# Kernel optimization log

Hardware: AMD Instinct MI355X
Metric: run time of the kernel (lower is better)

Reference implementation:

```python
import jax, jax.numpy as jnp
import numpy as np

B, S, D = 2, 2048, 4096
NH, NKV, HD = 32, 8, 128
NREP = NH // NKV
ROPE_THETA = 10000.0


def setup_inputs() -> dict:
    key = jax.random.key(0)
    k1, k2, k3, k4, k5 = jax.random.split(key, 5)
    x = jax.random.normal(k1, (B, S, D), jnp.float32)
    wq = jax.random.normal(k2, (NH * HD, D), jnp.float32) * 0.02
    wk = jax.random.normal(k3, (NKV * HD, D), jnp.float32) * 0.02
    wv = jax.random.normal(k4, (NKV * HD, D), jnp.float32) * 0.02
    wo = jax.random.normal(k5, (D, NH * HD), jnp.float32) * 0.02
    inv_freq = 1.0 / (ROPE_THETA ** (np.arange(0, HD, 2, dtype=np.float64) / HD))
    ang = np.outer(np.arange(S, dtype=np.float64), inv_freq)  # [S, HD/2]
    return {
        'x': x, 'start_pos': 0,
        'freqs_cos': jnp.asarray(np.cos(ang), jnp.float32),
        'freqs_sin': jnp.asarray(np.sin(ang), jnp.float32),
        'wq': wq, 'wk': wk, 'wv': wv, 'wo': wo,
    }


def _apply_rope(x, cos, sin):
    # x: [B, S, H, HD]; cos/sin: [S, HD/2]. Matches torch view_as_complex on
    # interleaved (even, odd) feature pairs: (xr + i*xi) * (cos + i*sin).
    xr = x[..., 0::2]
    xi = x[..., 1::2]
    c = cos[None, :, None, :]
    s = sin[None, :, None, :]
    out_r = xr * c - xi * s
    out_i = xr * s + xi * c
    return jnp.stack([out_r, out_i], axis=-1).reshape(x.shape)


def reference(x, start_pos, freqs_cos, freqs_sin, wq, wk, wv, wo):
    b, s, _ = x.shape
    xq = (x @ wq.T).reshape(b, s, NH, HD)
    xk = (x @ wk.T).reshape(b, s, NKV, HD)
    xv = (x @ wv.T).reshape(b, s, NKV, HD)
    # Source applies RoPE to K and V (not Q) -- reproduced faithfully.
    xk = _apply_rope(xk, freqs_cos, freqs_sin)
    xv = _apply_rope(xv, freqs_cos, freqs_sin)
    # start_pos == 0 prefill: cache slice [:, :start_pos+s] == freshly written xk/xv.
    # repeat_kv: head h_out = h_kv * NREP + rep  ==  jnp.repeat along head axis.
    keys = jnp.repeat(xk, NREP, axis=2)    # [B, S, NH, HD]
    values = jnp.repeat(xv, NREP, axis=2)  # [B, S, NH, HD]
    scale = 1.0 / jnp.sqrt(jnp.asarray(HD, x.dtype))
    scores = jnp.einsum('bqhd,bkhd->bhqk', xq, keys) * scale  # [B, NH, S, S]
    probs = jax.nn.softmax(scores, axis=-1)  # NOTE: no causal mask in source
    out = jnp.einsum('bhqk,bkhd->bqhd', probs, values).reshape(b, s, NH * HD)
    return out @ wo.T
```

## Files before the change

### kernel.cpp

```cpp
#include <hip/hip_runtime.h>
#include <hip/hip_bf16.h>


typedef short bf16x8 __attribute__((ext_vector_type(8)));
typedef float f32x4 __attribute__((ext_vector_type(4)));

__device__ __forceinline__ void load16(const void* g, void* l) {
  __builtin_amdgcn_global_load_lds(
      (const __attribute__((address_space(1))) void*)g,
      (__attribute__((address_space(3))) void*)l, 16, 0, 0);
}

__device__ __forceinline__ f32x4 mfma16(bf16x8 a, bf16x8 b, f32x4 c) {
  return __builtin_amdgcn_mfma_f32_16x16x32_bf16(a, b, c, 0, 0, 0);
}

__device__ __forceinline__ unsigned short f2b(float f) {
  union { float f; unsigned int u; } v; v.f = f;
  unsigned int u = v.u;
  return (unsigned short)((u + 0x7fffu + ((u >> 16) & 1u)) >> 16);
}
__device__ __forceinline__ float b2f(unsigned short u) {
  union { unsigned int u; float f; } v; v.u = ((unsigned int)u) << 16;
  return v.f;
}
__device__ __forceinline__ unsigned short f2b_fast(float f) {
  __hip_bfloat16 h = __float2bfloat16(f);
  return *reinterpret_cast<unsigned short*>(&h);
}

#define QSCALE (0.08838834764831845f * 1.4426950408889634f)

__global__ __launch_bounds__(256) void cvt_f32_bf16(
    const float* __restrict__ in, unsigned short* __restrict__ out, int n4) {
  int idx = blockIdx.x * 256 + threadIdx.x;
  int stride = gridDim.x * 256;
  for (int i = idx; i < n4; i += stride) {
    float4 v = reinterpret_cast<const float4*>(in)[i];
    ushort4 o;
    o.x = f2b(v.x); o.y = f2b(v.y); o.z = f2b(v.z); o.w = f2b(v.w);
    reinterpret_cast<ushort4*>(out)[i] = o;
  }
}

template <typename OutT>
__global__ __launch_bounds__(512, 2) void gemm256(
    const unsigned short* __restrict__ A, const unsigned short* __restrict__ Bw,
    OutT* __restrict__ C, int M, int N, int K, int sbl) {
  extern __shared__ char smem[];
  const int tid = threadIdx.x;
  const int lane = tid & 63;
  const int w = tid >> 6;
  const int lr = lane & 15, lg = lane >> 4;
  const int wr = w >> 2, wc = w & 3;

  const int nbn = N >> 8;
  const int bid = blockIdx.x, nwg = gridDim.x;
  const int swz = (bid & 7) * (nwg >> 3) + (bid >> 3);
  const int bm = swz / nbn, bn = swz % nbn;

  const unsigned short* Ag = A + (size_t)bm * 256 * K;
  const unsigned short* Bg = Bw + (size_t)bn * 256 * K;

  int srow[4], skhw[4], sdst[4];
#pragma unroll
  for (int j = 0; j < 4; ++j) {
    const int c = tid + j * 512;
    srow[j] = c >> 3;
    skhw[j] = ((c & 7) ^ ((c >> 3) & 7)) << 3;
    sdst[j] = ((tid & ~63) << 4) + j * 8192;
  }

  f32x4 acc[8][4];
#pragma unroll
  for (int m = 0; m < 8; ++m)
#pragma unroll
    for (int n = 0; n < 4; ++n) acc[m][n] = (f32x4){0.f, 0.f, 0.f, 0.f};

#define STAGEA4(tt)                                                           \
  {                                                                           \
    char* d = smem + (((tt)&1) * 65536);                                      \
    _Pragma("unroll") for (int j = 0; j < 4; ++j)                             \
        load16(Ag + (size_t)srow[j] * K + ((tt) << 6) + skhw[j], d + sdst[j]);\
  }
#define STAGEB4(tt)                                                           \
  {                                                                           \
    char* d = smem + (((tt)&1) * 65536) + 32768;                              \
    _Pragma("unroll") for (int j = 0; j < 4; ++j)                             \
        load16(Bg + (size_t)srow[j] * K + ((tt) << 6) + skhw[j], d + sdst[j]);\
  }

  STAGEB4(0);
  STAGEA4(0);

  const int NT = K >> 6;
  const int rx = (lr & 7) << 4;
  const int aRow0 = (wr * 128 + lr) * 128;
  const int bRow0 = (wc * 64 + lr) * 128;
  const int col0 = (lg * 16) ^ rx;
  const int col1 = (64 + lg * 16) ^ rx;

  bf16x8 aR[4][2], bR[4][2];

  for (int t = 0; t < NT; ++t) {
    const char* bufA = smem + (t & 1) * 65536;
    const char* bufB = bufA + 32768;
    const bool more = (t + 1) < NT;

    asm volatile("s_waitcnt vmcnt(0)" ::: "memory");
    __builtin_amdgcn_s_barrier();

#pragma unroll
    for (int mf = 0; mf < 4; ++mf) {
      aR[mf][0] = *(const bf16x8*)(bufA + aRow0 + mf * 2048 + col0);
      aR[mf][1] = *(const bf16x8*)(bufA + aRow0 + mf * 2048 + col1);
    }
#pragma unroll
    for (int nf = 0; nf < 2; ++nf) {
      bR[nf][0] = *(const bf16x8*)(bufB + bRow0 + nf * 2048 + col0);
      bR[nf][1] = *(const bf16x8*)(bufB + bRow0 + nf * 2048 + col1);
    }
    if (more) STAGEB4(t + 1);
    asm volatile("s_waitcnt lgkmcnt(8)" ::: "memory");
    __builtin_amdgcn_s_barrier();
    asm volatile("s_waitcnt lgkmcnt(0)" ::: "memory");
    __builtin_amdgcn_sched_barrier(0);
    __builtin_amdgcn_s_setprio(1);
#pragma unroll
    for (int mf = 0; mf < 4; ++mf)
#pragma unroll
      for (int nf = 0; nf < 2; ++nf) {
        acc[mf][nf] = mfma16(aR[mf][0], bR[nf][0], acc[mf][nf]);
        acc[mf][nf] = mfma16(aR[mf][1], bR[nf][1], acc[mf][nf]);
      }
    __builtin_amdgcn_s_setprio(0);
    __builtin_amdgcn_s_barrier();

#pragma unroll
    for (int nf = 2; nf < 4; ++nf) {
      bR[nf][0] = *(const bf16x8*)(bufB + bRow0 + nf * 2048 + col0);
      bR[nf][1] = *(const bf16x8*)(bufB + bRow0 + nf * 2048 + col1);
    }
    if (more) STAGEA4(t + 1);
    __builtin_amdgcn_s_barrier();
    asm volatile("s_waitcnt lgkmcnt(0)" ::: "memory");
    __builtin_amdgcn_sched_barrier(0);
    __builtin_amdgcn_s_setprio(1);
#pragma unroll
    for (int mf = 0; mf < 4; ++mf)
#pragma unroll
      for (int nf = 2; nf < 4; ++nf) {
        acc[mf][nf] = mfma16(aR[mf][0], bR[nf][0], acc[mf][nf]);
        acc[mf][nf] = mfma16(aR[mf][1], bR[nf][1], acc[mf][nf]);
      }
    __builtin_amdgcn_s_setprio(0);
    __builtin_amdgcn_s_barrier();

#pragma unroll
    for (int mf = 0; mf < 4; ++mf) {
      aR[mf][0] = *(const bf16x8*)(bufA + aRow0 + (4 + mf) * 2048 + col0);
      aR[mf][1] = *(const bf16x8*)(bufA + aRow0 + (4 + mf) * 2048 + col1);
    }
    __builtin_amdgcn_s_barrier();
    asm volatile("s_waitcnt lgkmcnt(0)" ::: "memory");
    __builtin_amdgcn_sched_barrier(0);
    __builtin_amdgcn_s_setprio(1);
#pragma unroll
    for (int mf = 0; mf < 4; ++mf)
#pragma unroll
      for (int nf = 0; nf < 2; ++nf) {
        acc[4 + mf][nf] = mfma16(aR[mf][0], bR[nf][0], acc[4 + mf][nf]);
        acc[4 + mf][nf] = mfma16(aR[mf][1], bR[nf][1], acc[4 + mf][nf]);
      }
    __builtin_amdgcn_s_setprio(0);
    __builtin_amdgcn_s_barrier();

    __builtin_amdgcn_s_setprio(1);
#pragma unroll
    for (int mf = 0; mf < 4; ++mf)
#pragma unroll
      for (int nf = 2; nf < 4; ++nf) {
        acc[4 + mf][nf] = mfma16(aR[mf][0], bR[nf][0], acc[4 + mf][nf]);
        acc[4 + mf][nf] = mfma16(aR[mf][1], bR[nf][1], acc[4 + mf][nf]);
      }
    __builtin_amdgcn_s_setprio(0);
  }
#undef STAGEA4
#undef STAGEB4

  const float cscale = (bn < sbl) ? QSCALE : 1.0f;
#pragma unroll
  for (int mf = 0; mf < 8; ++mf)
#pragma unroll
    for (int nf = 0; nf < 4; ++nf)
#pragma unroll
      for (int r = 0; r < 4; ++r) {
        int rowc = bm * 256 + wr * 128 + mf * 16 + lg * 4 + r;
        int colc = bn * 256 + wc * 64 + nf * 16 + lr;
        float v = acc[mf][nf][r] * cscale;
        if constexpr (sizeof(OutT) == 2)
          C[(size_t)rowc * N + colc] = (OutT)f2b(v);
        else
          C[(size_t)rowc * N + colc] = v;
      }
}

__global__ __launch_bounds__(256) void rope_kv(
    const unsigned short* __restrict__ XQKV,
    const float* __restrict__ fc, const float* __restrict__ fs,
    unsigned short* __restrict__ Kr, unsigned short* __restrict__ Vt) {
  __shared__ unsigned short Vl[128][66];
  const int t = threadIdx.x;
  const int bid = blockIdx.x;
  const int stile = bid & 31, bkv = bid >> 5;
  const int b = bkv >> 3, kvh = bkv & 7;
  const int s0 = stile * 64;
  const int l = t & 63;
  const int jrow = t >> 6;

  for (int j = 0; j < 16; ++j) {
    int s = s0 + j * 4 + jrow;
    ushort2 v = *(const ushort2*)(XQKV + (size_t)(b * 2048 + s) * 6144 + 4096 +
                                  kvh * 128 + 2 * l);
    float c = fc[s * 64 + l], sn = fs[s * 64 + l];
    float xr = b2f(v.x), xi = b2f(v.y);
    ushort2 o;
    o.x = f2b(xr * c - xi * sn);
    o.y = f2b(xr * sn + xi * c);
    *(ushort2*)(Kr + ((size_t)bkv * 2048 + s) * 128 + 2 * l) = o;
  }
  for (int j = 0; j < 16; ++j) {
    int ss = j * 4 + jrow;
    int s = s0 + ss;
    ushort2 v = *(const ushort2*)(XQKV + (size_t)(b * 2048 + s) * 6144 + 5120 +
                                  kvh * 128 + 2 * l);
    float c = fc[s * 64 + l], sn = fs[s * 64 + l];
    float xr = b2f(v.x), xi = b2f(v.y);
    Vl[2 * l][ss] = f2b(xr * c - xi * sn);
    Vl[2 * l + 1][ss] = f2b(xr * sn + xi * c);
  }
  __syncthreads();
  const int d = t >> 1, half = t & 1;
  unsigned short* vdst = Vt + ((size_t)bkv * 128 + d) * 2048 + s0 + half * 32;
#pragma unroll
  for (int e = 0; e < 32; e += 4) {
    ushort4 pk;
    pk.x = Vl[d][half * 32 + e];
    pk.y = Vl[d][half * 32 + e + 1];
    pk.z = Vl[d][half * 32 + e + 2];
    pk.w = Vl[d][half * 32 + e + 3];
    *(ushort4*)(vdst + e) = pk;
  }
}

__global__ __launch_bounds__(256, 2) void attn_fwd(
    const unsigned short* __restrict__ XQ, const unsigned short* __restrict__ Kr,
    const unsigned short* __restrict__ Vt, unsigned short* __restrict__ AO) {
  extern __shared__ char smem[];
  char* Ksm = smem;
  char* Vsm = smem + 16384;
  unsigned short* Ps = (unsigned short*)(smem + 32768);
  const int t = threadIdx.x;
  const int lane = t & 63, w = t >> 6;
  const int lr = lane & 15, lg = lane >> 4;

  const int bid = blockIdx.x;
  const int nwg = gridDim.x;
  const int swz = (bid & 7) * (nwg >> 3) + (bid >> 3);
  const int qt = swz & 7;
  const int bh = swz >> 3;
  const int b = bh >> 5, h = bh & 31;
  const int bkv = b * 8 + (h >> 2);

  bf16x8 qf[4][4];
#pragma unroll
  for (int q4 = 0; q4 < 4; ++q4) {
    const unsigned short* qp =
        XQ + ((size_t)(b * 2048 + qt * 256 + w * 64 + q4 * 16 + lr)) * 6144 +
        h * 128 + lg * 8;
#pragma unroll
    for (int dc = 0; dc < 4; ++dc) qf[q4][dc] = *(const bf16x8*)(qp + dc * 32);
  }

  f32x4 acc[4][8];
#pragma unroll
  for (int q4 = 0; q4 < 4; ++q4)
#pragma unroll
    for (int i = 0; i < 8; ++i) acc[q4][i] = (f32x4){0.f, 0.f, 0.f, 0.f};
  float l_[4][4];
#pragma unroll
  for (int q4 = 0; q4 < 4; ++q4)
#pragma unroll
    for (int r = 0; r < 4; ++r) l_[q4][r] = 0.f;

  const unsigned short* Kbase = Kr + (size_t)bkv * 2048 * 128;
  const unsigned short* Vbase = Vt + (size_t)bkv * 128 * 2048;

  const int c0 = t, c1 = t + 256;
  const int kK0 = c0 & 31, dC0 = c0 >> 5;
  const int kK1 = c1 & 31, dC1 = c1 >> 5;
  const int vD0 = c0 & 127, vKc0 = c0 >> 7;
  const int vD1 = c1 & 127, vKc1 = c1 >> 7;
  const int dstb0 = (c0 & ~63) * 16;
  const int dstb1 = (c1 & ~63) * 16;

#define STAGE_KV(bufi, kt)                                                     \
  {                                                                            \
    char* kd = Ksm + (bufi)*8192;                                              \
    char* vd = Vsm + (bufi)*8192;                                              \
    load16(Kbase + (size_t)((kt)*32 + kK0) * 128 + dC0 * 8, kd + dstb0);       \
    load16(Kbase + (size_t)((kt)*32 + kK1) * 128 + dC1 * 8, kd + dstb1);       \
    load16(Vbase + (size_t)vD0 * 2048 + (kt)*32 + vKc0 * 8, vd + dstb0);       \
    load16(Vbase + (size_t)vD1 * 2048 + (kt)*32 + vKc1 * 8, vd + dstb1);       \
  }

  STAGE_KV(0, 0);
  asm volatile("s_waitcnt vmcnt(0)" ::: "memory");
  __builtin_amdgcn_s_barrier();

  unsigned short* Pw = Ps + w * 2048;
  const int pbase = (lr >> 3) * 512 + (lr & 7);

  for (int kt = 0; kt < 64; ++kt) {
    const int cur = kt & 1;
    if (kt < 63) STAGE_KV(cur ^ 1, kt + 1);

    const char* Kc = Ksm + cur * 8192;
    const char* Vc = Vsm + cur * 8192;

#pragma unroll
    for (int nf = 0; nf < 2; ++nf) {
      f32x4 s[4];
#pragma unroll
      for (int q4 = 0; q4 < 4; ++q4) s[q4] = (f32x4){0.f, 0.f, 0.f, 0.f};
#pragma unroll
      for (int dc = 0; dc < 4; ++dc) {
        bf16x8 kf =
            *(const bf16x8*)(Kc + ((dc * 4 + lg) * 32 + nf * 16 + lr) * 16);
#pragma unroll
        for (int q4 = 0; q4 < 4; ++q4) s[q4] = mfma16(qf[q4][dc], kf, s[q4]);
      }
      const int pb = pbase + nf * 1024;
#pragma unroll
      for (int q4 = 0; q4 < 4; ++q4)
#pragma unroll
        for (int r = 0; r < 4; ++r) {
          float p = __builtin_amdgcn_exp2f(s[q4][r]);
          l_[q4][r] += p;
          Pw[pb + (q4 * 16 + lg * 4 + r) * 8] = f2b_fast(p);
        }
    }

    bf16x8 pf[4];
#pragma unroll
    for (int q4 = 0; q4 < 4; ++q4)
      pf[q4] = *(const bf16x8*)(Pw + lg * 512 + (q4 * 16 + lr) * 8);
#pragma unroll
    for (int dt = 0; dt < 8; ++dt) {
      bf16x8 vf = *(const bf16x8*)(Vc + (lg * 128 + dt * 16 + lr) * 16);
#pragma unroll
      for (int q4 = 0; q4 < 4; ++q4)
        acc[q4][dt] = mfma16(pf[q4], vf, acc[q4][dt]);
    }

    asm volatile("s_waitcnt vmcnt(0)" ::: "memory");
    __builtin_amdgcn_s_barrier();
  }
#undef STAGE_KV

#pragma unroll
  for (int q4 = 0; q4 < 4; ++q4)
#pragma unroll
    for (int r = 0; r < 4; ++r) {
#pragma unroll
      for (int o = 1; o < 16; o <<= 1) l_[q4][r] += __shfl_xor(l_[q4][r], o);
    }

#pragma unroll
  for (int q4 = 0; q4 < 4; ++q4)
#pragma unroll
    for (int r = 0; r < 4; ++r) {
      float inv = 1.f / l_[q4][r];
      size_t rowb =
          ((size_t)(b * 2048 + qt * 256 + w * 64 + q4 * 16 + lg * 4 + r)) * 4096 +
          h * 128;
#pragma unroll
      for (int dt = 0; dt < 8; ++dt)
        AO[rowb + dt * 16 + lr] = f2b_fast(acc[q4][dt][r] * inv);
    }
}

extern "C" void kernel_launch(void* const* d_in, const int* in_sizes, int n_in,
                              void* d_out, int out_size, void* d_ws, size_t ws_size,
                              hipStream_t stream) {
  const float* x  = (const float*)d_in[0];
  const float* fc = (const float*)d_in[2];
  const float* fs = (const float*)d_in[3];
  const float* wq = (const float*)d_in[4];
  const float* wk = (const float*)d_in[5];
  const float* wv = (const float*)d_in[6];
  const float* wo = (const float*)d_in[7];

  const size_t MB = 1024ull * 1024ull;
  char* ws = (char*)d_ws;
  unsigned short* Xb   = (unsigned short*)(ws);
  unsigned short* Wsc  = (unsigned short*)(ws + 32 * MB);
  unsigned short* Kr   = (unsigned short*)(ws);
  unsigned short* Vt   = (unsigned short*)(ws + 8 * MB);
  unsigned short* AO   = (unsigned short*)(ws + 80 * MB);
  unsigned short* XQKV = (unsigned short*)d_out;

  (void)hipFuncSetAttribute((const void*)gemm256<unsigned short>,
                            hipFuncAttributeMaxDynamicSharedMemorySize, 131072);
  (void)hipFuncSetAttribute((const void*)gemm256<float>,
                            hipFuncAttributeMaxDynamicSharedMemorySize, 131072);
  (void)hipFuncSetAttribute((const void*)attn_fwd,
                            hipFuncAttributeMaxDynamicSharedMemorySize, 49152);

  dim3 blk(256);
  dim3 blk512(512);
  cvt_f32_bf16<<<2048, blk, 0, stream>>>(x, Xb, (2 * 2048 * 4096) / 4);
  cvt_f32_bf16<<<2048, blk, 0, stream>>>(wq, Wsc, (4096 * 4096) / 4);
  cvt_f32_bf16<<<2048, blk, 0, stream>>>(wk, Wsc + 4096 * 4096, (1024 * 4096) / 4);
  cvt_f32_bf16<<<2048, blk, 0, stream>>>(wv, Wsc + 5120 * 4096, (1024 * 4096) / 4);
  gemm256<unsigned short><<<384, blk512, 131072, stream>>>(
      Xb, Wsc, XQKV, 4096, 6144, 4096, 16);
  rope_kv<<<512, blk, 0, stream>>>(XQKV, fc, fs, Kr, Vt);
  attn_fwd<<<512, blk, 49152, stream>>>(XQKV, Kr, Vt, AO);
  cvt_f32_bf16<<<2048, blk, 0, stream>>>(wo, Wsc, (4096 * 4096) / 4);
  gemm256<float><<<256, blk512, 131072, stream>>>(
      AO, Wsc, (float*)d_out, 4096, 4096, 4096, 0);
}
```

Baseline: 564.7 us.

## Deepen GEMM prefetch pipeline with split-half staging and partial vmcnt waits

Rewrites the GEMM main loop to process two K-tiles per iteration. Global-to-LDS loads are split into half-tile chunks issued between MFMA phases, and the full vmcnt(0) drain is replaced with vmcnt(10) gates so more loads stay in flight. B rows are remapped so each wave's 32-column slices land contiguously in LDS halves. Redundant wraparound loads (te/to fallback to tiles 0/1) are issued at the end, and the layout reasoning is fragile: vmcnt counting and buffer reuse must be exactly right or results break.

Result: faster. 542.9 us (-3.9%).

```diff
diff --git a/kernel.cpp b/kernel.cpp
--- a/kernel.cpp
+++ b/kernel.cpp
@@ -62,131 +62,207 @@
   const unsigned short* Ag = A + (size_t)bm * 256 * K;
   const unsigned short* Bg = Bw + (size_t)bn * 256 * K;
 
-  int srow[4], skhw[4], sdst[4];
+  int aoffs[4], boffs[4], sdst[4];
 #pragma unroll
   for (int j = 0; j < 4; ++j) {
     const int c = tid + j * 512;
-    srow[j] = c >> 3;
-    skhw[j] = ((c & 7) ^ ((c >> 3) & 7)) << 3;
+    const int u = c >> 3;
+    const int slot = ((c & 7) ^ (u & 7)) << 3;
+    aoffs[j] = u * K + slot;
+    const int br = ((u & 127) >> 5) * 64 + (u >> 7) * 32 + (u & 31);
+    boffs[j] = br * K + slot;
     sdst[j] = ((tid & ~63) << 4) + j * 8192;
   }
 
-  f32x4 acc[8][4];
-#pragma unroll
-  for (int m = 0; m < 8; ++m)
-#pragma unroll
-    for (int n = 0; n < 4; ++n) acc[m][n] = (f32x4){0.f, 0.f, 0.f, 0.f};
-
-#define STAGEA4(tt)                                                           \
+#define ST_A(hh, tt)                                                          \
   {                                                                           \
     char* d = smem + (((tt)&1) * 65536);                                      \
-    _Pragma("unroll") for (int j = 0; j < 4; ++j)                             \
-        load16(Ag + (size_t)srow[j] * K + ((tt) << 6) + skhw[j], d + sdst[j]);\
-  }
-#define STAGEB4(tt)                                                           \
+    load16(Ag + aoffs[(hh)] + ((tt) << 6), d + sdst[(hh)]);                   \
+    load16(Ag + aoffs[(hh) + 2] + ((tt) << 6), d + sdst[(hh) + 2]);           \
+  }
+#define ST_B(hh, tt)                                                          \
   {                                                                           \
     char* d = smem + (((tt)&1) * 65536) + 32768;                              \
-    _Pragma("unroll") for (int j = 0; j < 4; ++j)                             \
-        load16(Bg + (size_t)srow[j] * K + ((tt) << 6) + skhw[j], d + sdst[j]);\
-  }
-
-  STAGEB4(0);
-  STAGEA4(0);
+    load16(Bg + boffs[(hh)*2] + ((tt) << 6), d + sdst[(hh)*2]);               \
+    load16(Bg + boffs[(hh)*2 + 1] + ((tt) << 6), d + sdst[(hh)*2 + 1]);       \
+  }
+#define GATE10                                                                \
+  asm volatile("s_waitcnt vmcnt(10)" ::: "memory");                           \
+  __builtin_amdgcn_s_barrier();
+#define LGKM0                                                                 \
+  asm volatile("s_waitcnt lgkmcnt(0)" ::: "memory");                          \
+  __builtin_amdgcn_sched_barrier(0);
+
+  f32x4 acc[8][4];
+#pragma unroll
+  for (int m = 0; m < 8; ++m)
+#pragma unroll
+    for (int n = 0; n < 4; ++n) acc[m][n] = (f32x4){0.f, 0.f, 0.f, 0.f};
+
+  ST_A(0, 0); ST_B(0, 0); ST_B(1, 0); ST_A(1, 0);
+  ST_A(0, 1); ST_B(0, 1); ST_B(1, 1);
 
   const int NT = K >> 6;
-  const int rx = (lr & 7) << 4;
-  const int aRow0 = (wr * 128 + lr) * 128;
-  const int bRow0 = (wc * 64 + lr) * 128;
-  const int col0 = (lg * 16) ^ rx;
-  const int col1 = (64 + lg * 16) ^ rx;
-
-  bf16x8 aR[4][2], bR[4][2];
-
-  for (int t = 0; t < NT; ++t) {
-    const char* bufA = smem + (t & 1) * 65536;
-    const char* bufB = bufA + 32768;
-    const bool more = (t + 1) < NT;
-
-    asm volatile("s_waitcnt vmcnt(0)" ::: "memory");
-    __builtin_amdgcn_s_barrier();
-
+  const int NI = NT >> 1;
+  const int xr = (lr & 7) << 4;
+  const int aBase = (wr * 128 + lr) * 128;
+  const int bBase = (wc * 32 + lr) * 128;
+  const int col0 = (lg * 16) ^ xr;
+  const int col1 = (64 + lg * 16) ^ xr;
+
+  bf16x8 aR[4][2], b01[2][2], b23[2][2];
+
+  for (int i = 0; i < NI; ++i) {
+    const int T1 = 2 * i + 1;
+    const int te = (2 * i + 2 < NT) ? 2 * i + 2 : 0;
+    const int to = (2 * i + 3 < NT) ? 2 * i + 3 : 1;
+    const char* d0 = smem;
+    const char* d1 = smem + 65536;
+
+    GATE10;
 #pragma unroll
     for (int mf = 0; mf < 4; ++mf) {
-      aR[mf][0] = *(const bf16x8*)(bufA + aRow0 + mf * 2048 + col0);
-      aR[mf][1] = *(const bf16x8*)(bufA + aRow0 + mf * 2048 + col1);
+      aR[mf][0] = *(const bf16x8*)(d0 + aBase + mf * 2048 + col0);
+      aR[mf][1] = *(const bf16x8*)(d0 + aBase + mf * 2048 + col1);
     }
 #pragma unroll
     for (int nf = 0; nf < 2; ++nf) {
-      bR[nf][0] = *(const bf16x8*)(bufB + bRow0 + nf * 2048 + col0);
-      bR[nf][1] = *(const bf16x8*)(bufB + bRow0 + nf * 2048 + col1);
-    }
-    if (more) STAGEB4(t + 1);
-    asm volatile("s_waitcnt lgkmcnt(8)" ::: "memory");
-    __builtin_amdgcn_s_barrier();
-    asm volatile("s_waitcnt lgkmcnt(0)" ::: "memory");
-    __builtin_amdgcn_sched_barrier(0);
-    __builtin_amdgcn_s_setprio(1);
-#pragma unroll
-    for (int mf = 0; mf < 4; ++mf)
-#pragma unroll
-      for (int nf = 0; nf < 2; ++nf) {
-        acc[mf][nf] = mfma16(aR[mf][0], bR[nf][0], acc[mf][nf]);
-        acc[mf][nf] = mfma16(aR[mf][1], bR[nf][1], acc[mf][nf]);
-      }
-    __builtin_amdgcn_s_setprio(0);
-    __builtin_amdgcn_s_barrier();
-
-#pragma unroll
-    for (int nf = 2; nf < 4; ++nf) {
-      bR[nf][0] = *(const bf16x8*)(bufB + bRow0 + nf * 2048 + col0);
-      bR[nf][1] = *(const bf16x8*)(bufB + bRow0 + nf * 2048 + col1);
-    }
-    if (more) STAGEA4(t + 1);
-    __builtin_amdgcn_s_barrier();
-    asm volatile("s_waitcnt lgkmcnt(0)" ::: "memory");
-    __builtin_amdgcn_sched_barrier(0);
-    __builtin_amdgcn_s_setprio(1);
-#pragma unroll
-    for (int mf = 0; mf < 4; ++mf)
-#pragma unroll
-      for (int nf = 2; nf < 4; ++nf) {
-        acc[mf][nf] = mfma16(aR[mf][0], bR[nf][0], acc[mf][nf]);
-        acc[mf][nf] = mfma16(aR[mf][1], bR[nf][1], acc[mf][nf]);
-      }
-    __builtin_amdgcn_s_setprio(0);
-    __builtin_amdgcn_s_barrier();
-
+      b01[nf][0] = *(const bf16x8*)(d0 + 32768 + bBase + nf * 2048 + col0);
+      b01[nf][1] = *(const bf16x8*)(d0 + 32768 + bBase + nf * 2048 + col1);
+    }
+    ST_A(1, T1);
+    LGKM0;
+    __builtin_amdgcn_s_setprio(1);
+#pragma unroll
+    for (int mf = 0; mf < 4; ++mf)
+#pragma unroll
+      for (int nf = 0; nf < 2; ++nf) {
+        acc[mf][nf] = mfma16(aR[mf][0], b01[nf][0], acc[mf][nf]);
+        acc[mf][nf] = mfma16(aR[mf][1], b01[nf][1], acc[mf][nf]);
+      }
+    __builtin_amdgcn_s_setprio(0);
+
+    GATE10;
+#pragma unroll
+    for (int nf = 0; nf < 2; ++nf) {
+      b23[nf][0] = *(const bf16x8*)(d0 + 32768 + 16384 + bBase + nf * 2048 + col0);
+      b23[nf][1] = *(const bf16x8*)(d0 + 32768 + 16384 + bBase + nf * 2048 + col1);
+    }
+    ST_A(0, te);
+    LGKM0;
+    __builtin_amdgcn_s_setprio(1);
+#pragma unroll
+    for (int mf = 0; mf < 4; ++mf)
+#pragma unroll
+      for (int nf = 0; nf < 2; ++nf) {
+        acc[mf][2 + nf] = mfma16(aR[mf][0], b23[nf][0], acc[mf][2 + nf]);
+        acc[mf][2 + nf] = mfma16(aR[mf][1], b23[nf][1], acc[mf][2 + nf]);
+      }
+    __builtin_amdgcn_s_setprio(0);
+
+    GATE10;
 #pragma unroll
     for (int mf = 0; mf < 4; ++mf) {
-      aR[mf][0] = *(const bf16x8*)(bufA + aRow0 + (4 + mf) * 2048 + col0);
-      aR[mf][1] = *(const bf16x8*)(bufA + aRow0 + (4 + mf) * 2048 + col1);
-    }
-    __builtin_amdgcn_s_barrier();
-    asm volatile("s_waitcnt lgkmcnt(0)" ::: "memory");
-    __builtin_amdgcn_sched_barrier(0);
-    __builtin_amdgcn_s_setprio(1);
-#pragma unroll
-    for (int mf = 0; mf < 4; ++mf)
-#pragma unroll
-      for (int nf = 0; nf < 2; ++nf) {
-        acc[4 + mf][nf] = mfma16(aR[mf][0], bR[nf][0], acc[4 + mf][nf]);
-        acc[4 + mf][nf] = mfma16(aR[mf][1], bR[nf][1], acc[4 + mf][nf]);
-      }
-    __builtin_amdgcn_s_setprio(0);
-    __builtin_amdgcn_s_barrier();
-
-    __builtin_amdgcn_s_setprio(1);
-#pragma unroll
-    for (int mf = 0; mf < 4; ++mf)
-#pragma unroll
-      for (int nf = 2; nf < 4; ++nf) {
-        acc[4 + mf][nf] = mfma16(aR[mf][0], bR[nf][0], acc[4 + mf][nf]);
-        acc[4 + mf][nf] = mfma16(aR[mf][1], bR[nf][1], acc[4 + mf][nf]);
-      }
-    __builtin_amdgcn_s_setprio(0);
-  }
-#undef STAGEA4
-#undef STAGEB4
+      aR[mf][0] = *(const bf16x8*)(d0 + aBase + (4 + mf) * 2048 + col0);
+      aR[mf][1] = *(const bf16x8*)(d0 + aBase + (4 + mf) * 2048 + col1);
+    }
+    ST_B(0, te);
+    LGKM0;
+    __builtin_amdgcn_s_setprio(1);
+#pragma unroll
+    for (int mf = 0; mf < 4; ++mf)
+#pragma unroll
+      for (int nf = 0; nf < 2; ++nf) {
+        acc[4 + mf][nf] = mfma16(aR[mf][0], b01[nf][0], acc[4 + mf][nf]);
+        acc[4 + mf][nf] = mfma16(aR[mf][1], b01[nf][1], acc[4 + mf][nf]);
+      }
+    __builtin_amdgcn_s_setprio(0);
+
+    ST_B(1, te);
+    __builtin_amdgcn_s_setprio(1);
+#pragma unroll
+    for (int mf = 0; mf < 4; ++mf)
+#pragma unroll
+      for (int nf = 0; nf < 2; ++nf) {
+        acc[4 + mf][2 + nf] = mfma16(aR[mf][0], b23[nf][0], acc[4 + mf][2 + nf]);
+        acc[4 + mf][2 + nf] = mfma16(aR[mf][1], b23[nf][1], acc[4 + mf][2 + nf]);
+      }
+    __builtin_amdgcn_s_setprio(0);
+
+    GATE10;
+#pragma unroll
+    for (int mf = 0; mf < 4; ++mf) {
+      aR[mf][0] = *(const bf16x8*)(d1 + aBase + mf * 2048 + col0);
+      aR[mf][1] = *(const bf16x8*)(d1 + aBase + mf * 2048 + col1);
+    }
+#pragma unroll
+    for (int nf = 0; nf < 2; ++nf) {
+      b01[nf][0] = *(const bf16x8*)(d1 + 32768 + bBase + nf * 2048 + col0);
+      b01[nf][1] = *(const bf16x8*)(d1 + 32768 + bBase + nf * 2048 + col1);
+    }
+    ST_A(1, te);
+    LGKM0;
+    __builtin_amdgcn_s_setprio(1);
+#pragma unroll
+    for (int mf = 0; mf < 4; ++mf)
+#pragma unroll
+      for (int nf = 0; nf < 2; ++nf) {
+        acc[mf][nf] = mfma16(aR[mf][0], b01[nf][0], acc[mf][nf]);
+        acc[mf][nf] = mfma16(aR[mf][1], b01[nf][1], acc[mf][nf]);
+      }
+    __builtin_amdgcn_s_setprio(0);
+
+    GATE10;
+#pragma unroll
+    for (int nf = 0; nf < 2; ++nf) {
+      b23[nf][0] = *(const bf16x8*)(d1 + 32768 + 16384 + bBase + nf * 2048 + col0);
+      b23[nf][1] = *(const bf16x8*)(d1 + 32768 + 16384 + bBase + nf * 2048 + col1);
+    }
+    ST_A(0, to);
+    LGKM0;
+    __builtin_amdgcn_s_setprio(1);
+#pragma unroll
+    for (int mf = 0; mf < 4; ++mf)
+#pragma unroll
+      for (int nf = 0; nf < 2; ++nf) {
+        acc[mf][2 + nf] = mfma16(aR[mf][0], b23[nf][0], acc[mf][2 + nf]);
+        acc[mf][2 + nf] = mfma16(aR[mf][1], b23[nf][1], acc[mf][2 + nf]);
+      }
+    __builtin_amdgcn_s_setprio(0);
+
+    GATE10;
+#pragma unroll
+    for (int mf = 0; mf < 4; ++mf) {
+      aR[mf][0] = *(const bf16x8*)(d1 + aBase + (4 + mf) * 2048 + col0);
+      aR[mf][1] = *(const bf16x8*)(d1 + aBase + (4 + mf) * 2048 + col1);
+    }
+    ST_B(0, to);
+    LGKM0;
+    __builtin_amdgcn_s_setprio(1);
+#pragma unroll
+    for (int mf = 0; mf < 4; ++mf)
+#pragma unroll
+      for (int nf = 0; nf < 2; ++nf) {
+        acc[4 + mf][nf] = mfma16(aR[mf][0], b01[nf][0], acc[4 + mf][nf]);
+        acc[4 + mf][nf] = mfma16(aR[mf][1], b01[nf][1], acc[4 + mf][nf]);
+      }
+    __builtin_amdgcn_s_setprio(0);
+
+    ST_B(1, to);
+    __builtin_amdgcn_s_setprio(1);
+#pragma unroll
+    for (int mf = 0; mf < 4; ++mf)
+#pragma unroll
+      for (int nf = 0; nf < 2; ++nf) {
+        acc[4 + mf][2 + nf] = mfma16(aR[mf][0], b23[nf][0], acc[4 + mf][2 + nf]);
+        acc[4 + mf][2 + nf] = mfma16(aR[mf][1], b23[nf][1], acc[4 + mf][2 + nf]);
+      }
+    __builtin_amdgcn_s_setprio(0);
+  }
+#undef ST_A
+#undef ST_B
+#undef GATE10
+#undef LGKM0
 
   const float cscale = (bn < sbl) ? QSCALE : 1.0f;
 #pragma unroll
```
